# Optimization experiments

Hardware: AMD Instinct MI355X
Metric: run time of the kernel (lower is better)

The kernel has to match this reference:

```python
import jax, jax.numpy as jnp
import numpy as np

LN2 = 0.69314718  # matches the 2ln2 constant in the original rbf()


def setup_inputs() -> dict:
    key = jax.random.key(0)
    domain_min = [-1.0, -1.0, -1.0]
    domain_max = [1.0, 1.0, 1.0]
    n = [12, 12, 12]
    codomain_dim = 128
    N = 200000

    axes = [jnp.linspace(domain_min[i], domain_max[i], n[i], dtype=jnp.float32)
            for i in range(len(n))]
    # torch.meshgrid default is 'ij' indexing
    grid = jnp.stack(jnp.meshgrid(*axes, indexing='ij'), axis=-1).reshape(-1, len(n))  # [G, 3]

    # rbf_width: mean nearest-neighbor distance on the grid (second-smallest per row)
    d = jnp.linalg.norm(grid[:, None, :] - grid[None, :, :], axis=-1)  # [G, G], G=1728 -> small
    width = jnp.sort(d, axis=1)[:, 1].mean()

    # interpolation matrix m and coeffs = solve(m, weight), as in __init__ (no_grad buffer)
    m = jnp.exp(-(d ** 2) / (width ** 2 / LN2))
    k1, k2 = jax.random.split(key)
    weight = jax.random.normal(k1, (grid.shape[0], codomain_dim), dtype=jnp.float32)
    coeffs = jnp.linalg.solve(m, weight)  # [G, C]

    x = jax.random.normal(k2, (N, len(n)), dtype=jnp.float32)  # [N, 3]
    return {"x": x, "grid": grid, "coeffs": coeffs, "width": width}


def reference(x, grid, coeffs, width):
    # Squared Euclidean distance via |a|^2 + |b|^2 - 2ab (avoids [N, G, 3] broadcast tensor).
    # rbf(d, w) = exp(-d^2 / (w^2 / ln2)); since it only uses d^2, skip the sqrt.
    x2 = jnp.sum(x * x, axis=-1, keepdims=True)          # [N, 1]
    g2 = jnp.sum(grid * grid, axis=-1)                   # [G]
    d2 = x2 + g2[None, :] - 2.0 * (x @ grid.T)           # [N, G]
    d2 = jnp.maximum(d2, 0.0)                            # numerical guard
    p = jnp.exp(-d2 * (LN2 / (width * width)))           # [N, G]
    return p @ coeffs                                    # [N, C]
```

## Files before the change

### kernel.cpp

```cpp
#include <hip/hip_runtime.h>
#include <stdint.h>


typedef _Float16 f16;
typedef _Float16 f16x8 __attribute__((ext_vector_type(8)));
typedef float f32x16 __attribute__((ext_vector_type(16)));

#define LN2F 0.69314718f
#define LOG2E 1.4426950408889634f

#define CD 128
#define KD 1728

__global__ void prep_coeffs(const float* __restrict__ coeffs,
                            f16* __restrict__ img) {
  int kp  = blockIdx.x * 2 + (threadIdx.x >> 7);
  int col = threadIdx.x & 127;
  int i   = kp / 144;
  int r   = kp - i * 144;
  int s   = r >> 4;
  int idx = r & 15;
  int hh  = idx >> 3;
  int b   = idx & 7;
  int j, k2;
  if (s < 6) { j = 2 * s + hh;                 k2 = b; }
  else       { j = 4 * (s - 6) + 2 * hh + (b >> 2); k2 = 8 + (b & 3); }
  float v = coeffs[(size_t)((i * 12 + j) * 12 + k2) * CD + col];
  f16 h = (f16)v;
  f16 l = (f16)(v - (float)h);
  int q   = i * 9 + s;
  int ch2 = col >> 6;
  int c64 = col & 63;
  size_t o = (size_t)q * 4096 + ch2 * 2048 + hh * 512 + c64 * 8 + b;
  img[o]        = h;
  img[o + 1024] = l;
}

union FU { uint32_t u[4]; f16x8 v; };

__global__ __launch_bounds__(256) void rbf_gemm(
    const float* __restrict__ x,
    const float* __restrict__ width,
    const f16* __restrict__ img,
    float* __restrict__ out, int N) {
  const int t    = threadIdx.x;
  const int lane = t & 63;
  const int wv   = t >> 6;
  const int l31  = lane & 31;
  const int hh   = lane >> 5;
  const int rbase = blockIdx.x * 256;
  const int ch2   = blockIdx.y;

  const float w  = width[0];
  const float s2 = (LN2F * LOG2E) / (w * w);

  int r0 = rbase + wv * 64 + l31;      if (r0 >= N) r0 = N - 1;
  int r1 = rbase + wv * 64 + 32 + l31; if (r1 >= N) r1 = N - 1;
  const float x00 = x[(size_t)r0 * 3 + 0];
  const float x01 = x[(size_t)r0 * 3 + 1];
  const float x02 = x[(size_t)r0 * 3 + 2];
  const float x10 = x[(size_t)r1 * 3 + 0];
  const float x11 = x[(size_t)r1 * 3 + 1];
  const float x12 = x[(size_t)r1 * 3 + 2];

  float e1a[2][12], e2a[2][12];
#pragma unroll
  for (int k = 0; k < 12; ++k) {
    float g = (float)k * (2.0f / 11.0f) - 1.0f;
    float d;
    d = x01 - g; e1a[0][k] = __builtin_amdgcn_exp2f(-d * d * s2);
    d = x11 - g; e1a[1][k] = __builtin_amdgcn_exp2f(-d * d * s2);
    d = x02 - g; e2a[0][k] = __builtin_amdgcn_exp2f(-d * d * s2);
    d = x12 - g; e2a[1][k] = __builtin_amdgcn_exp2f(-d * d * s2);
  }

  const int voff = ch2 * 4096 + hh * 1024 + l31 * 16;
  const char* imgb = (const char*)img;

  f16x8 B0[4], B1[4], B2[4];
#pragma unroll
  for (int f = 0; f < 4; ++f) {
    const int off = (f & 1) * 512 + (f >> 1) * 2048;
    B0[f] = *(const f16x8*)(imgb + voff + off);
    B1[f] = *(const f16x8*)(imgb + 8192 + voff + off);
  }

  f32x16 acc00, acc01, acc10, acc11;
#pragma unroll
  for (int q = 0; q < 16; ++q) { acc00[q] = 0.f; acc01[q] = 0.f; acc10[q] = 0.f; acc11[q] = 0.f; }

#pragma unroll 1
  for (int i = 0; i < 12; ++i) {
    float gi = (float)i * (2.0f / 11.0f) - 1.0f;
    float d0;
    d0 = x00 - gi; float e00 = __builtin_amdgcn_exp2f(-d0 * d0 * s2);
    d0 = x10 - gi; float e01v = __builtin_amdgcn_exp2f(-d0 * d0 * s2);

#pragma unroll
    for (int s = 0; s < 9; ++s) {
      f16x8* CUR = (s % 3 == 0) ? B0 : (s % 3 == 1) ? B1 : B2;
      f16x8* NXT = (s % 3 == 0) ? B2 : (s % 3 == 1) ? B0 : B1;

      float es0, es1, c010, c230, c011, c231;
      if (s < 6) {
        es0 = e00  * (hh ? e1a[0][2 * s + 1] : e1a[0][2 * s]);
        es1 = e01v * (hh ? e1a[1][2 * s + 1] : e1a[1][2 * s]);
      } else {
        int J0 = 4 * (s - 6);
        c010 = e00  * (hh ? e1a[0][J0 + 2] : e1a[0][J0 + 0]);
        c230 = e00  * (hh ? e1a[0][J0 + 3] : e1a[0][J0 + 1]);
        c011 = e01v * (hh ? e1a[1][J0 + 2] : e1a[1][J0 + 0]);
        c231 = e01v * (hh ? e1a[1][J0 + 3] : e1a[1][J0 + 1]);
      }

      FU ah0, al0, ah1, al1;
#pragma unroll
      for (int q = 0; q < 4; ++q) {
        float ea0, eb0, ea1, eb1, esa0, esa1;
        if (s < 6) {
          ea0 = e2a[0][2 * q];     eb0 = e2a[0][2 * q + 1];
          ea1 = e2a[1][2 * q];     eb1 = e2a[1][2 * q + 1];
          esa0 = es0; esa1 = es1;
        } else {
          ea0 = e2a[0][8 + 2 * (q & 1)];  eb0 = e2a[0][9 + 2 * (q & 1)];
          ea1 = e2a[1][8 + 2 * (q & 1)];  eb1 = e2a[1][9 + 2 * (q & 1)];
          esa0 = (q < 2) ? c010 : c230;
          esa1 = (q < 2) ? c011 : c231;
        }
        uint32_t h0, h1;
        asm("v_fma_mixlo_f16 %0, %1, %2, 0" : "=v"(h0) : "v"(esa0), "v"(ea0));
        asm("v_fma_mixhi_f16 %0, %1, %2, 0" : "+v"(h0) : "v"(esa0), "v"(eb0));
        asm("v_fma_mixlo_f16 %0, %1, %2, 0" : "=v"(h1) : "v"(esa1), "v"(ea1));
        asm("v_fma_mixhi_f16 %0, %1, %2, 0" : "+v"(h1) : "v"(esa1), "v"(eb1));
        ah0.u[q] = h0;
        ah1.u[q] = h1;
      }

      __builtin_amdgcn_s_setprio(1);
      acc00 = __builtin_amdgcn_mfma_f32_32x32x16_f16(ah0.v, CUR[0], acc00, 0, 0, 0);
      acc01 = __builtin_amdgcn_mfma_f32_32x32x16_f16(ah0.v, CUR[1], acc01, 0, 0, 0);
      acc10 = __builtin_amdgcn_mfma_f32_32x32x16_f16(ah1.v, CUR[0], acc10, 0, 0, 0);
      acc11 = __builtin_amdgcn_mfma_f32_32x32x16_f16(ah1.v, CUR[1], acc11, 0, 0, 0);
      __builtin_amdgcn_s_setprio(0);

#pragma unroll
      for (int q = 0; q < 4; ++q) {
        float ea0, eb0, ea1, eb1, esa0, esa1;
        if (s < 6) {
          ea0 = e2a[0][2 * q];     eb0 = e2a[0][2 * q + 1];
          ea1 = e2a[1][2 * q];     eb1 = e2a[1][2 * q + 1];
          esa0 = es0; esa1 = es1;
        } else {
          ea0 = e2a[0][8 + 2 * (q & 1)];  eb0 = e2a[0][9 + 2 * (q & 1)];
          ea1 = e2a[1][8 + 2 * (q & 1)];  eb1 = e2a[1][9 + 2 * (q & 1)];
          esa0 = (q < 2) ? c010 : c230;
          esa1 = (q < 2) ? c011 : c231;
        }
        uint32_t l0, l1;
        uint32_t h0 = ah0.u[q], h1 = ah1.u[q];
        asm("v_fma_mixlo_f16 %0, %1, %2, -%3 op_sel:[0,0,0] op_sel_hi:[0,0,1]"
            : "=v"(l0) : "v"(esa0), "v"(ea0), "v"(h0));
        asm("v_fma_mixhi_f16 %0, %1, %2, -%3 op_sel:[0,0,1] op_sel_hi:[0,0,1]"
            : "+v"(l0) : "v"(esa0), "v"(eb0), "v"(h0));
        asm("v_fma_mixlo_f16 %0, %1, %2, -%3 op_sel:[0,0,0] op_sel_hi:[0,0,1]"
            : "=v"(l1) : "v"(esa1), "v"(ea1), "v"(h1));
        asm("v_fma_mixhi_f16 %0, %1, %2, -%3 op_sel:[0,0,1] op_sel_hi:[0,0,1]"
            : "+v"(l1) : "v"(esa1), "v"(eb1), "v"(h1));
        al0.u[q] = l0;
        al1.u[q] = l1;
      }

      __builtin_amdgcn_s_setprio(1);
      acc00 = __builtin_amdgcn_mfma_f32_32x32x16_f16(al0.v, CUR[0], acc00, 0, 0, 0);
      acc01 = __builtin_amdgcn_mfma_f32_32x32x16_f16(al0.v, CUR[1], acc01, 0, 0, 0);
      acc10 = __builtin_amdgcn_mfma_f32_32x32x16_f16(al1.v, CUR[0], acc10, 0, 0, 0);
      acc11 = __builtin_amdgcn_mfma_f32_32x32x16_f16(al1.v, CUR[1], acc11, 0, 0, 0);
      __builtin_amdgcn_s_setprio(0);

      {
        const char* spn = imgb + (size_t)(i * 9 + s + 2) * 8192;
#pragma unroll
        for (int f = 0; f < 4; ++f) {
          const int off = (f & 1) * 512 + (f >> 1) * 2048;
          NXT[f] = *(const f16x8*)(spn + voff + off);
        }
      }

      __builtin_amdgcn_s_setprio(1);
      acc00 = __builtin_amdgcn_mfma_f32_32x32x16_f16(ah0.v, CUR[2], acc00, 0, 0, 0);
      acc01 = __builtin_amdgcn_mfma_f32_32x32x16_f16(ah0.v, CUR[3], acc01, 0, 0, 0);
      acc10 = __builtin_amdgcn_mfma_f32_32x32x16_f16(ah1.v, CUR[2], acc10, 0, 0, 0);
      acc11 = __builtin_amdgcn_mfma_f32_32x32x16_f16(ah1.v, CUR[3], acc11, 0, 0, 0);
      __builtin_amdgcn_s_setprio(0);
    }
  }

#pragma unroll
  for (int q = 0; q < 16; ++q) {
    int row0 = rbase + wv * 64 + (q & 3) + 8 * (q >> 2) + 4 * hh;
    int col  = ch2 * 64 + l31;
    if (row0 < N) {
      out[(size_t)row0 * CD + col]      = acc00[q];
      out[(size_t)row0 * CD + col + 32] = acc01[q];
    }
    int row1 = row0 + 32;
    if (row1 < N) {
      out[(size_t)row1 * CD + col]      = acc10[q];
      out[(size_t)row1 * CD + col + 32] = acc11[q];
    }
  }
}

__global__ void rbf_fallback(const float* __restrict__ x, const float* __restrict__ grid,
                             const float* __restrict__ coeffs, const float* __restrict__ width,
                             float* __restrict__ out, int N) {
  int row = blockIdx.x;
  int col = threadIdx.x;
  if (row >= N) return;
  float x0 = x[(size_t)row * 3 + 0];
  float x1 = x[(size_t)row * 3 + 1];
  float x2 = x[(size_t)row * 3 + 2];
  float w = width[0];
  float s2 = (LN2F * LOG2E) / (w * w);
  float acc = 0.f;
  for (int g = 0; g < 1728; ++g) {
    float d0 = x0 - grid[g * 3 + 0];
    float d1 = x1 - grid[g * 3 + 1];
    float d2 = x2 - grid[g * 3 + 2];
    float p = exp2f(-(d0 * d0 + d1 * d1 + d2 * d2) * s2);
    acc += p * coeffs[(size_t)g * CD + col];
  }
  out[(size_t)row * CD + col] = acc;
}

extern "C" void kernel_launch(void* const* d_in, const int* in_sizes, int n_in,
                              void* d_out, int out_size, void* d_ws, size_t ws_size,
                              hipStream_t stream) {
  const float* x      = (const float*)d_in[0];
  const float* grid   = (const float*)d_in[1];
  const float* coeffs = (const float*)d_in[2];
  const float* width  = (const float*)d_in[3];
  float* out = (float*)d_out;
  int N = in_sizes[0] / 3;

  size_t need = (size_t)108 * 8192 + 2 * 8192;
  if (ws_size >= need) {
    f16* img = (f16*)d_ws;
    hipLaunchKernelGGL(prep_coeffs, dim3(KD / 2), dim3(256), 0, stream,
                       coeffs, img);
    int nb = (N + 255) / 256;
    hipLaunchKernelGGL(rbf_gemm, dim3(nb, 2), dim3(256), 0, stream,
                       x, width, img, out, N);
  } else {
    hipLaunchKernelGGL(rbf_fallback, dim3(N), dim3(CD), 0, stream,
                       x, grid, coeffs, width, out, N);
  }
}
```

Before: 251.8 us.

## Move per-row exp tables to LDS and shrink B prefetch to one stage

Stores the separable exp factors for the first two coordinates in shared memory instead of per-thread register arrays, and cuts the coefficient prefetch from triple buffering to a single next-step buffer. Launch bounds now request four blocks per SM. The aim is to lower VGPR pressure so more waves can hide latency. The cost is extra LDS reads each inner step, a block barrier, and a shorter prefetch distance that may expose global load latency.

```diff
diff --git a/kernel.cpp b/kernel.cpp
--- a/kernel.cpp
+++ b/kernel.cpp
@@ -11,6 +11,7 @@
 
 #define CD 128
 #define KD 1728
+#define BM 256
 
 __global__ void prep_coeffs(const float* __restrict__ coeffs,
                             f16* __restrict__ img) {
@@ -38,52 +39,64 @@
 
 union FU { uint32_t u[4]; f16x8 v; };
 
-__global__ __launch_bounds__(256) void rbf_gemm(
+__global__ __launch_bounds__(256, 4) void rbf_gemm(
     const float* __restrict__ x,
     const float* __restrict__ width,
     const f16* __restrict__ img,
     float* __restrict__ out, int N) {
+  __shared__ float E0[12 * BM];
+  __shared__ float E1[12 * BM];
+
   const int t    = threadIdx.x;
   const int lane = t & 63;
   const int wv   = t >> 6;
   const int l31  = lane & 31;
   const int hh   = lane >> 5;
-  const int rbase = blockIdx.x * 256;
+  const int rbase = blockIdx.x * BM;
   const int ch2   = blockIdx.y;
 
   const float w  = width[0];
   const float s2 = (LN2F * LOG2E) / (w * w);
 
-  int r0 = rbase + wv * 64 + l31;      if (r0 >= N) r0 = N - 1;
-  int r1 = rbase + wv * 64 + 32 + l31; if (r1 >= N) r1 = N - 1;
-  const float x00 = x[(size_t)r0 * 3 + 0];
-  const float x01 = x[(size_t)r0 * 3 + 1];
-  const float x02 = x[(size_t)r0 * 3 + 2];
-  const float x10 = x[(size_t)r1 * 3 + 0];
-  const float x11 = x[(size_t)r1 * 3 + 1];
-  const float x12 = x[(size_t)r1 * 3 + 2];
-
-  float e1a[2][12], e2a[2][12];
-#pragma unroll
-  for (int k = 0; k < 12; ++k) {
-    float g = (float)k * (2.0f / 11.0f) - 1.0f;
-    float d;
-    d = x01 - g; e1a[0][k] = __builtin_amdgcn_exp2f(-d * d * s2);
-    d = x11 - g; e1a[1][k] = __builtin_amdgcn_exp2f(-d * d * s2);
-    d = x02 - g; e2a[0][k] = __builtin_amdgcn_exp2f(-d * d * s2);
-    d = x12 - g; e2a[1][k] = __builtin_amdgcn_exp2f(-d * d * s2);
+  {
+    int rr = rbase + t; if (rr >= N) rr = N - 1;
+    float x0 = x[(size_t)rr * 3 + 0];
+    float x1 = x[(size_t)rr * 3 + 1];
+#pragma unroll
+    for (int k = 0; k < 12; ++k) {
+      float g = (float)k * (2.0f / 11.0f) - 1.0f;
+      float d0 = x0 - g;
+      float d1 = x1 - g;
+      E0[k * BM + t] = __builtin_amdgcn_exp2f(-d0 * d0 * s2);
+      E1[k * BM + t] = __builtin_amdgcn_exp2f(-d1 * d1 * s2);
+    }
+  }
+
+  const int rl0 = wv * 64 + l31;
+  const int rl1 = rl0 + 32;
+
+  float e2a[2][12];
+#pragma unroll
+  for (int mi = 0; mi < 2; ++mi) {
+    int rr = rbase + (mi ? rl1 : rl0); if (rr >= N) rr = N - 1;
+    float x2v = x[(size_t)rr * 3 + 2];
+#pragma unroll
+    for (int k = 0; k < 12; ++k) {
+      float g = (float)k * (2.0f / 11.0f) - 1.0f;
+      float d = x2v - g;
+      e2a[mi][k] = __builtin_amdgcn_exp2f(-d * d * s2);
+    }
   }
 
   const int voff = ch2 * 4096 + hh * 1024 + l31 * 16;
   const char* imgb = (const char*)img;
 
-  f16x8 B0[4], B1[4], B2[4];
-#pragma unroll
-  for (int f = 0; f < 4; ++f) {
-    const int off = (f & 1) * 512 + (f >> 1) * 2048;
-    B0[f] = *(const f16x8*)(imgb + voff + off);
-    B1[f] = *(const f16x8*)(imgb + 8192 + voff + off);
-  }
+  f16x8 cb0 = *(const f16x8*)(imgb + voff + 0);
+  f16x8 cb1 = *(const f16x8*)(imgb + voff + 512);
+  f16x8 cb2 = *(const f16x8*)(imgb + voff + 2048);
+  f16x8 cb3 = *(const f16x8*)(imgb + voff + 2560);
+
+  __syncthreads();
 
   f32x16 acc00, acc01, acc10, acc11;
 #pragma unroll
@@ -91,26 +104,33 @@
 
 #pragma unroll 1
   for (int i = 0; i < 12; ++i) {
-    float gi = (float)i * (2.0f / 11.0f) - 1.0f;
-    float d0;
-    d0 = x00 - gi; float e00 = __builtin_amdgcn_exp2f(-d0 * d0 * s2);
-    d0 = x10 - gi; float e01v = __builtin_amdgcn_exp2f(-d0 * d0 * s2);
+    float e0m0 = E0[i * BM + rl0];
+    float e0m1 = E0[i * BM + rl1];
 
 #pragma unroll
     for (int s = 0; s < 9; ++s) {
-      f16x8* CUR = (s % 3 == 0) ? B0 : (s % 3 == 1) ? B1 : B2;
-      f16x8* NXT = (s % 3 == 0) ? B2 : (s % 3 == 1) ? B0 : B1;
-
       float es0, es1, c010, c230, c011, c231;
       if (s < 6) {
-        es0 = e00  * (hh ? e1a[0][2 * s + 1] : e1a[0][2 * s]);
-        es1 = e01v * (hh ? e1a[1][2 * s + 1] : e1a[1][2 * s]);
+        float ej00 = e0m0 * E1[(2 * s + 0) * BM + rl0];
+        float ej01 = e0m0 * E1[(2 * s + 1) * BM + rl0];
+        float ej10 = e0m1 * E1[(2 * s + 0) * BM + rl1];
+        float ej11 = e0m1 * E1[(2 * s + 1) * BM + rl1];
+        es0 = hh ? ej01 : ej00;
+        es1 = hh ? ej11 : ej10;
       } else {
         int J0 = 4 * (s - 6);
-        c010 = e00  * (hh ? e1a[0][J0 + 2] : e1a[0][J0 + 0]);
-        c230 = e00  * (hh ? e1a[0][J0 + 3] : e1a[0][J0 + 1]);
-        c011 = e01v * (hh ? e1a[1][J0 + 2] : e1a[1][J0 + 0]);
-        c231 = e01v * (hh ? e1a[1][J0 + 3] : e1a[1][J0 + 1]);
+        float ej00 = e0m0 * E1[(J0 + 0) * BM + rl0];
+        float ej01 = e0m0 * E1[(J0 + 1) * BM + rl0];
+        float ej02 = e0m0 * E1[(J0 + 2) * BM + rl0];
+        float ej03 = e0m0 * E1[(J0 + 3) * BM + rl0];
+        float ej10 = e0m1 * E1[(J0 + 0) * BM + rl1];
+        float ej11 = e0m1 * E1[(J0 + 1) * BM + rl1];
+        float ej12 = e0m1 * E1[(J0 + 2) * BM + rl1];
+        float ej13 = e0m1 * E1[(J0 + 3) * BM + rl1];
+        c010 = hh ? ej02 : ej00;
+        c230 = hh ? ej03 : ej01;
+        c011 = hh ? ej12 : ej10;
+        c231 = hh ? ej13 : ej11;
       }
 
       FU ah0, al0, ah1, al1;
@@ -137,11 +157,17 @@
       }
 
       __builtin_amdgcn_s_setprio(1);
-      acc00 = __builtin_amdgcn_mfma_f32_32x32x16_f16(ah0.v, CUR[0], acc00, 0, 0, 0);
-      acc01 = __builtin_amdgcn_mfma_f32_32x32x16_f16(ah0.v, CUR[1], acc01, 0, 0, 0);
-      acc10 = __builtin_amdgcn_mfma_f32_32x32x16_f16(ah1.v, CUR[0], acc10, 0, 0, 0);
-      acc11 = __builtin_amdgcn_mfma_f32_32x32x16_f16(ah1.v, CUR[1], acc11, 0, 0, 0);
+      acc00 = __builtin_amdgcn_mfma_f32_32x32x16_f16(ah0.v, cb0, acc00, 0, 0, 0);
+      acc01 = __builtin_amdgcn_mfma_f32_32x32x16_f16(ah0.v, cb1, acc01, 0, 0, 0);
+      acc10 = __builtin_amdgcn_mfma_f32_32x32x16_f16(ah1.v, cb0, acc10, 0, 0, 0);
+      acc11 = __builtin_amdgcn_mfma_f32_32x32x16_f16(ah1.v, cb1, acc11, 0, 0, 0);
       __builtin_amdgcn_s_setprio(0);
+
+      const char* spn = imgb + (size_t)(i * 9 + s + 1) * 8192;
+      f16x8 nb0 = *(const f16x8*)(spn + voff + 0);
+      f16x8 nb1 = *(const f16x8*)(spn + voff + 512);
+      f16x8 nb2 = *(const f16x8*)(spn + voff + 2048);
+      f16x8 nb3 = *(const f16x8*)(spn + voff + 2560);
 
 #pragma unroll
       for (int q = 0; q < 4; ++q) {
@@ -171,27 +197,18 @@
       }
 
       __builtin_amdgcn_s_setprio(1);
-      acc00 = __builtin_amdgcn_mfma_f32_32x32x16_f16(al0.v, CUR[0], acc00, 0, 0, 0);
-      acc01 = __builtin_amdgcn_mfma_f32_32x32x16_f16(al0.v, CUR[1], acc01, 0, 0, 0);
-      acc10 = __builtin_amdgcn_mfma_f32_32x32x16_f16(al1.v, CUR[0], acc10, 0, 0, 0);
-      acc11 = __builtin_amdgcn_mfma_f32_32x32x16_f16(al1.v, CUR[1], acc11, 0, 0, 0);
+      acc00 = __builtin_amdgcn_mfma_f32_32x32x16_f16(al0.v, cb0, acc00, 0, 0, 0);
+      acc01 = __builtin_amdgcn_mfma_f32_32x32x16_f16(al0.v, cb1, acc01, 0, 0, 0);
+      acc10 = __builtin_amdgcn_mfma_f32_32x32x16_f16(al1.v, cb0, acc10, 0, 0, 0);
+      acc11 = __builtin_amdgcn_mfma_f32_32x32x16_f16(al1.v, cb1, acc11, 0, 0, 0);
+
+      acc00 = __builtin_amdgcn_mfma_f32_32x32x16_f16(ah0.v, cb2, acc00, 0, 0, 0);
+      acc01 = __builtin_amdgcn_mfma_f32_32x32x16_f16(ah0.v, cb3, acc01, 0, 0, 0);
+      acc10 = __builtin_amdgcn_mfma_f32_32x32x16_f16(ah1.v, cb2, acc10, 0, 0, 0);
+      acc11 = __builtin_amdgcn_mfma_f32_32x32x16_f16(ah1.v, cb3, acc11, 0, 0, 0);
       __builtin_amdgcn_s_setprio(0);
 
-      {
-        const char* spn = imgb + (size_t)(i * 9 + s + 2) * 8192;
-#pragma unroll
-        for (int f = 0; f < 4; ++f) {
-          const int off = (f & 1) * 512 + (f >> 1) * 2048;
-          NXT[f] = *(const f16x8*)(spn + voff + off);
-        }
-      }
-
-      __builtin_amdgcn_s_setprio(1);
-      acc00 = __builtin_amdgcn_mfma_f32_32x32x16_f16(ah0.v, CUR[2], acc00, 0, 0, 0);
-      acc01 = __builtin_amdgcn_mfma_f32_32x32x16_f16(ah0.v, CUR[3], acc01, 0, 0, 0);
-      acc10 = __builtin_amdgcn_mfma_f32_32x32x16_f16(ah1.v, CUR[2], acc10, 0, 0, 0);
-      acc11 = __builtin_amdgcn_mfma_f32_32x32x16_f16(ah1.v, CUR[3], acc11, 0, 0, 0);
-      __builtin_amdgcn_s_setprio(0);
+      cb0 = nb0; cb1 = nb1; cb2 = nb2; cb3 = nb3;
     }
   }
 
@@ -248,7 +265,7 @@
     f16* img = (f16*)d_ws;
     hipLaunchKernelGGL(prep_coeffs, dim3(KD / 2), dim3(256), 0, stream,
                        coeffs, img);
-    int nb = (N + 255) / 256;
+    int nb = (N + BM - 1) / BM;
     hipLaunchKernelGGL(rbf_gemm, dim3(nb, 2), dim3(256), 0, stream,
                        x, width, img, out, N);
   } else {
```

Result: slower. 799.2 us (+217.4%).
